# Optimization experiments

Measured on AMD Instinct MI355X. Metric: run time of the kernel, lower is better.

Reference implementation:

```python
import jax, jax.numpy as jnp
import numpy as np

N = 50000      # nodes
E = 800000     # edges (before self-loops)
IN_DIM = 128
HID = 64
OUT = 32
HEADS = 8
BN_EPS = 1e-5
NEG_SLOPE = 0.2  # PyG GATConv default


def setup_inputs() -> dict:
    key = jax.random.key(0)
    ks = jax.random.split(key, 24)
    g = lambda k, shape, fan_in: (jax.random.normal(k, shape, jnp.float32) / np.sqrt(fan_in))
    return {
        "x": jax.random.normal(ks[0], (N, IN_DIM), jnp.float32),
        "edge_index": jax.random.randint(ks[1], (2, E), 0, N, dtype=jnp.int64),
        # GCN1
        "gcn1_w": g(ks[2], (IN_DIM, HID), IN_DIM),
        "gcn1_b": jnp.zeros((HID,), jnp.float32),
        # BN1 (eval mode running stats)
        "bn1_gamma": jnp.ones((HID,), jnp.float32),
        "bn1_beta": jnp.zeros((HID,), jnp.float32),
        "bn1_mean": 0.1 * jax.random.normal(ks[3], (HID,), jnp.float32),
        "bn1_var": 0.5 + jax.random.uniform(ks[4], (HID,), jnp.float32),
        # GAT1: heads=8, per-head out=HID, concat=False -> mean over heads
        "gat1_w": g(ks[5], (HID, HEADS * HID), HID),
        "gat1_asrc": g(ks[6], (HEADS, HID), HID),
        "gat1_adst": g(ks[7], (HEADS, HID), HID),
        "gat1_b": jnp.zeros((HID,), jnp.float32),
        # GCN2
        "gcn2_w": g(ks[8], (HID, HID), HID),
        "gcn2_b": jnp.zeros((HID,), jnp.float32),
        # BN2
        "bn2_gamma": jnp.ones((HID,), jnp.float32),
        "bn2_beta": jnp.zeros((HID,), jnp.float32),
        "bn2_mean": 0.1 * jax.random.normal(ks[9], (HID,), jnp.float32),
        "bn2_var": 0.5 + jax.random.uniform(ks[10], (HID,), jnp.float32),
        # GAT2: heads=8, per-head out=OUT, concat=False
        "gat2_w": g(ks[11], (HID, HEADS * OUT), HID),
        "gat2_asrc": g(ks[12], (HEADS, OUT), OUT),
        "gat2_adst": g(ks[13], (HEADS, OUT), OUT),
        "gat2_b": jnp.zeros((OUT,), jnp.float32),
    }


def _gcn(x, src, dst, w, b, n):
    # PyG GCNConv: x @ W, symmetric norm with self-loops (src/dst already include them)
    h = x @ w
    deg = jax.ops.segment_sum(jnp.ones(src.shape[0], x.dtype), dst, num_segments=n)
    dinv = jnp.where(deg > 0, jax.lax.rsqrt(jnp.maximum(deg, 1.0)), 0.0)
    coef = dinv[src] * dinv[dst]                     # [E']
    out = jax.ops.segment_sum(coef[:, None] * h[src], dst, num_segments=n)
    return out + b


def _gat(x, src, dst, w, a_src, a_dst, b, n, heads, ch):
    # PyG GATConv (concat=False): mean over heads, softmax over incoming edges per dst
    h = (x @ w).reshape(n, heads, ch)                # [N,H,C]
    es = jnp.einsum('nhc,hc->nh', h, a_src)          # alpha_src per node
    ed = jnp.einsum('nhc,hc->nh', h, a_dst)
    e = jax.nn.leaky_relu(es[src] + ed[dst], NEG_SLOPE)  # [E',H]
    m = jax.ops.segment_max(e, dst, num_segments=n)
    m = jnp.where(jnp.isfinite(m), m, 0.0)
    ex = jnp.exp(e - m[dst])
    denom = jax.ops.segment_sum(ex, dst, num_segments=n)
    alpha = ex / (denom[dst] + 1e-16)                # [E',H]
    out = jnp.zeros((n, ch), x.dtype)
    for hd in range(heads):  # fixed small head loop keeps peak edge memory at [E',C]
        msg = alpha[:, hd, None] * h[src, hd]        # [E',C]
        out = out + jax.ops.segment_sum(msg, dst, num_segments=n)
    return out / heads + b


def _bn_eval(x, gamma, beta, mean, var):
    return (x - mean) * jax.lax.rsqrt(var + BN_EPS) * gamma + beta


def reference(x, edge_index,
              gcn1_w, gcn1_b, bn1_gamma, bn1_beta, bn1_mean, bn1_var,
              gat1_w, gat1_asrc, gat1_adst, gat1_b,
              gcn2_w, gcn2_b, bn2_gamma, bn2_beta, bn2_mean, bn2_var,
              gat2_w, gat2_asrc, gat2_adst, gat2_b):
    n = x.shape[0]
    loops = jnp.arange(n, dtype=edge_index.dtype)
    src = jnp.concatenate([edge_index[0], loops])    # self-loops (PyG default)
    dst = jnp.concatenate([edge_index[1], loops])

    h = _gcn(x, src, dst, gcn1_w, gcn1_b, n)
    h = jax.nn.relu(_bn_eval(h, bn1_gamma, bn1_beta, bn1_mean, bn1_var))
    h = jax.nn.relu(_gat(h, src, dst, gat1_w, gat1_asrc, gat1_adst, gat1_b, n, HEADS, HID))
    h = _gcn(h, src, dst, gcn2_w, gcn2_b, n)
    h = jax.nn.relu(_bn_eval(h, bn2_gamma, bn2_beta, bn2_mean, bn2_var))
    h = _gat(h, src, dst, gat2_w, gat2_asrc, gat2_adst, gat2_b, n, HEADS, OUT)
    return jax.nn.log_softmax(h, axis=1)
```

## Files before the change

### kernel.cpp

```cpp
#include <hip/hip_runtime.h>
#include <hip/hip_bf16.h>

#define NN 50000
#define NE 800000
#define IND 128
#define NH 8
#define EBLK 256
#define EPB 3125
#define NBUK 391
#define NBUKP 392
#define GH (NBUKP * EBLK)
#define PREPB 308

typedef __hip_bfloat16 bf16;
typedef __attribute__((ext_vector_type(8))) short short8;
typedef __attribute__((ext_vector_type(8))) __bf16 bf16x8;
typedef __attribute__((ext_vector_type(4))) float floatx4;
typedef __attribute__((ext_vector_type(2))) float floatx2;

static __device__ __forceinline__ short f2bf_bits(float f) {
    unsigned u = __float_as_uint(f);
    u = (u + 0x7fffu + ((u >> 16) & 1u)) >> 16;
    return (short)u;
}
static __device__ __forceinline__ float bf2f(bf16 v) { return __bfloat162float(v); }
static __device__ __forceinline__ floatx2 up2(unsigned av) {
    floatx2 r;
    r.x = __uint_as_float(av << 16);
    r.y = __uint_as_float(av & 0xffff0000u);
    return r;
}
static __device__ __forceinline__ unsigned pk2(float a, float b) {
    return (unsigned)(unsigned short)f2bf_bits(a) | ((unsigned)(unsigned short)f2bf_bits(b) << 16);
}
static __device__ __forceinline__ void pk_fma_lo(floatx2& acc, floatx2 a, floatx2 al) {
    asm("v_pk_fma_f32 %0, %1, %2, %0 op_sel:[0,0,0] op_sel_hi:[1,0,1]"
        : "+v"(acc) : "v"(a), "v"(al));
}
static __device__ __forceinline__ void pk_fma_hi(floatx2& acc, floatx2 a, floatx2 al) {
    asm("v_pk_fma_f32 %0, %1, %2, %0 op_sel:[0,1,0] op_sel_hi:[1,1,1]"
        : "+v"(acc) : "v"(a), "v"(al));
}

static __device__ __forceinline__ void scan_buckets(const int* __restrict__ bsum,
        int* sp, int* gb, int tid) {
    int v0 = (2 * tid < NBUKP) ? bsum[2 * tid] : 0;
    int v1 = (2 * tid + 1 < NBUKP) ? bsum[2 * tid + 1] : 0;
    int c = v0 + v1;
    sp[tid] = c; __syncthreads();
    int val = c;
#pragma unroll
    for (int off = 1; off < 256; off <<= 1) {
        int t = (tid >= off) ? sp[tid - off] : 0;
        __syncthreads();
        val += t; sp[tid] = val;
        __syncthreads();
    }
    int pex = val - c;
    gb[2 * tid] = pex;
    gb[2 * tid + 1] = pex + v0;
    __syncthreads();
}

__global__ __launch_bounds__(256) void bin_count_prep_kernel(const int* __restrict__ edst,
        int* __restrict__ ghist,
        const float* __restrict__ gcn1_w, const float* __restrict__ gcn2_w,
        const float* __restrict__ gat1_w, const float* __restrict__ gat2_w,
        const float* __restrict__ as1, const float* __restrict__ ad1,
        const float* __restrict__ as2, const float* __restrict__ ad2,
        bf16* __restrict__ wT1, bf16* __restrict__ wT2,
        bf16* __restrict__ wgT1, bf16* __restrict__ wgT2,
        float* __restrict__ was1, float* __restrict__ wad1,
        float* __restrict__ was2, float* __restrict__ wad2) {
    __shared__ int hsh[NBUKP];
    const int tid = threadIdx.x;
    if (blockIdx.x < EBLK) {
        const int blk = blockIdx.x;
        for (int b = tid; b < NBUKP; b += 256) hsh[b] = 0;
        __syncthreads();
        const int e0 = blk * EPB;
        for (int e = e0 + tid; e < e0 + EPB; e += 256)
            atomicAdd(&hsh[edst[e] >> 7], 1);
        __syncthreads();
        for (int b = tid; b < NBUKP; b += 256)
            ghist[b * EBLK + blk] = hsh[b];
    } else {
        int idx = (blockIdx.x - EBLK) * 256 + tid;
        if (idx < 8192) {
            int m = idx >> 7, k = idx & 127;
            ((short*)wT1)[idx] = f2bf_bits(gcn1_w[(long)k * 64 + m]);
        } else if (idx < 12288) {
            int i = idx - 8192;
            int m = i >> 6, k = i & 63;
            ((short*)wT2)[i] = f2bf_bits(gcn2_w[(long)k * 64 + m]);
        } else if (idx < 45056) {
            int i = idx - 12288;
            int m = i >> 9, k = i & 511;
            int h = k >> 6, c = k & 63;
            ((short*)wgT1)[i] = f2bf_bits(gat1_w[(long)c * 512 + h * 64 + m]);
        } else if (idx < 77824) {
            int i = idx - 45056;
            int m = i >> 9, k = i & 511;
            int h = k >> 6, c = k & 63;
            ((short*)wgT2)[i] = (m < 32) ? f2bf_bits(gat2_w[(long)c * 256 + h * 32 + m]) : (short)0;
        } else if (idx < 78336) {
            int i = idx - 77824;
            int h = i >> 6, c = i & 63;
            const float* wrow = gat1_w + (long)c * 512 + h * 64;
            float s = 0.f, d = 0.f;
            for (int cc = 0; cc < 64; ++cc) {
                float w = wrow[cc];
                s += w * as1[h * 64 + cc];
                d += w * ad1[h * 64 + cc];
            }
            was1[i] = s; wad1[i] = d;
        } else if (idx < 78848) {
            int i = idx - 78336;
            int h = i >> 6, c = i & 63;
            const float* wrow = gat2_w + (long)c * 256 + h * 32;
            float s = 0.f, d = 0.f;
            for (int cc = 0; cc < 32; ++cc) {
                float w = wrow[cc];
                s += w * as2[h * 32 + cc];
                d += w * ad2[h * 32 + cc];
            }
            was2[i] = s; wad2[i] = d;
        }
    }
}

__global__ __launch_bounds__(256) void scang1_kernel(const int* __restrict__ src,
        int* __restrict__ pre, int* __restrict__ bsum, int n) {
    __shared__ int sh[256];
    const int tid = threadIdx.x;
    const int idx = blockIdx.x * 256 + tid;
    int c = (idx < n) ? src[idx] : 0;
    sh[tid] = c; __syncthreads();
    int val = c;
#pragma unroll
    for (int off = 1; off < 256; off <<= 1) {
        int t = (tid >= off) ? sh[tid - off] : 0;
        __syncthreads();
        val += t; sh[tid] = val;
        __syncthreads();
    }
    if (idx < n) pre[idx] = val - c;
    if (tid == 255) bsum[blockIdx.x] = val;
}

__global__ __launch_bounds__(256) void bin_scatter_kernel(const int* __restrict__ esrc,
        const int* __restrict__ edst, const int* __restrict__ gpre,
        const int* __restrict__ bsum, unsigned* __restrict__ ebuf) {
    __shared__ int cur[NBUKP];
    __shared__ int sp[256], gb[512];
    const int tid = threadIdx.x, blk = blockIdx.x;
    scan_buckets(bsum, sp, gb, tid);
    for (int b = tid; b < NBUKP; b += 256)
        cur[b] = gpre[b * EBLK + blk] + gb[b];
    __syncthreads();
    const int e0 = blk * EPB;
    for (int e = e0 + tid; e < e0 + EPB; e += 256) {
        int d = edst[e], s = esrc[e];
        int pos = atomicAdd(&cur[d >> 7], 1);
        ebuf[pos] = ((unsigned)(d & 127) << 16) | (unsigned)s;
    }
}

__global__ __launch_bounds__(256) void bucket_finalize_kernel(const unsigned* __restrict__ ebuf,
        const int* __restrict__ gpre, const int* __restrict__ bsum,
        int* __restrict__ rowptr, float* __restrict__ dinv, int* __restrict__ csrc) {
    __shared__ int lh[128], lcur[128], sc[256];
    __shared__ int sp[256], gb[512];
    const int bu = blockIdx.x, tid = threadIdx.x;
    scan_buckets(bsum, sp, gb, tid);
    const int seg_beg = gpre[bu * EBLK] + gb[bu];
    const int seg_end = gpre[(bu + 1) * EBLK] + gb[bu + 1];
    if (tid < 128) lh[tid] = 0;
    __syncthreads();
    for (int i = seg_beg + tid; i < seg_end; i += 256)
        atomicAdd(&lh[ebuf[i] >> 16], 1);
    __syncthreads();
    int c = (tid < 128) ? lh[tid] : 0;
    sc[tid] = c; __syncthreads();
    int val = c;
#pragma unroll
    for (int off = 1; off < 256; off <<= 1) {
        int t = (tid >= off) ? sc[tid - off] : 0;
        __syncthreads();
        val += t; sc[tid] = val;
        __syncthreads();
    }
    int excl = val - c;
    if (tid < 128) {
        lcur[tid] = excl;
        int node = bu * 128 + tid;
        if (node < NN) {
            rowptr[node] = seg_beg + excl;
            dinv[node] = rsqrtf((float)c + 1.f);
        }
    }
    if (bu == 0 && tid == 0) rowptr[NN] = NE;
    __syncthreads();
    for (int i = seg_beg + tid; i < seg_end; i += 256) {
        unsigned u = ebuf[i];
        int pos = atomicAdd(&lcur[u >> 16], 1);
        csrc[seg_beg + pos] = (int)(u & 0xffffu);
    }
}

template<int K, int EPI, bool AF32>
__global__ __launch_bounds__(256) void mm2_kernel(const void* __restrict__ A,
        const bf16* __restrict__ wT, void* __restrict__ C,
        const float* __restrict__ bias, const float* __restrict__ rowscale,
        int nrows, int M) {
    const int row0 = blockIdx.x * 64;
    const int tid = threadIdx.x;
    const int lane = tid & 63, wave = tid >> 6;
    const int lr = lane & 15, q = lane >> 4;
    const int row = row0 + wave * 16 + lr;
    const bool rok = row < nrows;
    constexpr int NC = 4;
    floatx4 acc[NC] = {};
#pragma unroll 4
    for (int k0 = 0; k0 < K; k0 += 32) {
        short8 av = {0, 0, 0, 0, 0, 0, 0, 0};
        if (rok) {
            if (AF32) {
                const float* apf = (const float*)A + (long)row * K + q * 8 + k0;
                floatx4 va = *(const floatx4*)apf;
                floatx4 vb = *(const floatx4*)(apf + 4);
#pragma unroll
                for (int j = 0; j < 4; ++j) { av[j] = f2bf_bits(va[j]); av[4 + j] = f2bf_bits(vb[j]); }
            } else {
                av = *(const short8*)((const short*)A + (long)row * K + q * 8 + k0);
            }
        }
        bf16x8 a = __builtin_bit_cast(bf16x8, av);
#pragma unroll
        for (int c = 0; c < NC; ++c) {
            bf16x8 b = __builtin_bit_cast(bf16x8,
                *(const short8*)((const short*)wT + (long)(c * 16 + lr) * K + k0 + q * 8));
            acc[c] = __builtin_amdgcn_mfma_f32_16x16x32_bf16(a, b, acc[c], 0, 0, 0);
        }
    }
#pragma unroll
    for (int c = 0; c < NC; ++c)
#pragma unroll
        for (int r = 0; r < 4; ++r) {
            int orow = row0 + wave * 16 + q * 4 + r;
            int col = c * 16 + lr;
            if (orow < nrows && col < M) {
                long o = (long)orow * M + col;
                float v = acc[c][r];
                if (EPI == 0) ((float*)C)[o] = v;
                else if (EPI == 2) {
                    v = v * 0.125f + bias[col];
                    ((bf16*)C)[o] = __float2bfloat16(fmaxf(v, 0.f));
                } else {
                    ((bf16*)C)[o] = __float2bfloat16(rowscale[orow] * v);
                }
            }
        }
}

__global__ __launch_bounds__(256) void gcn_fused_kernel(const int* __restrict__ rowptr,
        const int* __restrict__ csrc, const float* __restrict__ dinv,
        const bf16* __restrict__ hin, const float* __restrict__ b,
        const float* __restrict__ gamma, const float* __restrict__ beta,
        const float* __restrict__ mean, const float* __restrict__ var,
        bf16* __restrict__ actout) {
    const int node = blockIdx.x * 4 + (threadIdx.x >> 6);
    if (node >= NN) return;
    const int lane = threadIdx.x & 63;
    const int eslot = lane >> 5, cp = lane & 31;
    const unsigned cpo = 4u * (unsigned)cp;
    const int beg = __builtin_amdgcn_readfirstlane(rowptr[node]);
    const int end = __builtin_amdgcn_readfirstlane(rowptr[node + 1]);
    const float di = dinv[node];
    const int* csp = csrc + beg;
    floatx2 acc2 = {0.f, 0.f};
    const int dn = end - beg;
    const int kup = (dn + 15) & ~15;
    for (int k0 = 0; k0 < kup; k0 += 16) {
        int s_[8]; float w_[8];
#pragma unroll
        for (int u = 0; u < 8; ++u) {
            int k = k0 + 2 * u + eslot;
            int ok = k < dn;
            s_[u] = csp[ok ? k : 0];
            w_[u] = ok ? 1.f : 0.f;
        }
        unsigned av_[8];
#pragma unroll
        for (int u = 0; u < 8; ++u)
            av_[u] = *(const unsigned*)((const char*)hin + ((unsigned)s_[u] * 128u + cpo));
#pragma unroll
        for (int u = 0; u < 8; ++u) {
            floatx2 a2 = up2(av_[u]);
            acc2 += a2 * w_[u];
        }
    }
    acc2.x += __shfl_xor(acc2.x, 32);
    acc2.y += __shfl_xor(acc2.y, 32);
    {
        unsigned sv = *(const unsigned*)((const char*)hin + ((unsigned)node * 128u + cpo));
        acc2 += up2(sv);
    }
    int c0 = 2 * cp, c1 = c0 + 1;
    float x0 = acc2.x * di + b[c0];
    float x1 = acc2.y * di + b[c1];
    x0 = (x0 - mean[c0]) * rsqrtf(var[c0] + 1e-5f) * gamma[c0] + beta[c0];
    x1 = (x1 - mean[c1]) * rsqrtf(var[c1] + 1e-5f) * gamma[c1] + beta[c1];
    if (eslot == 0)
        *(unsigned*)((unsigned short*)actout + (long)node * 64 + c0) =
            pk2(fmaxf(x0, 0.f), fmaxf(x1, 0.f));
}

__global__ __launch_bounds__(256) void scores_kernel(const bf16* __restrict__ actb,
        const float* __restrict__ was, const float* __restrict__ wad,
        float* __restrict__ es, float* __restrict__ ed, int n) {
    const int node = blockIdx.x * 4 + (threadIdx.x >> 6);
    if (node >= n) return;
    const int lane = threadIdx.x & 63;
    const int h = lane >> 3, cg = lane & 7;
    short8 a8 = *(const short8*)((const short*)actb + (long)node * 64 + cg * 8);
    const float* wsp = was + h * 64 + cg * 8;
    const float* wdp = wad + h * 64 + cg * 8;
    floatx4 ws0 = *(const floatx4*)wsp, ws1 = *(const floatx4*)(wsp + 4);
    floatx4 wd0 = *(const floatx4*)wdp, wd1 = *(const floatx4*)(wdp + 4);
    float s = 0.f, d = 0.f;
#pragma unroll
    for (int j = 0; j < 4; ++j) {
        float v0 = bf2f(__builtin_bit_cast(bf16, a8[j]));
        float v1 = bf2f(__builtin_bit_cast(bf16, a8[4 + j]));
        s += v0 * ws0[j] + v1 * ws1[j];
        d += v0 * wd0[j] + v1 * wd1[j];
    }
#pragma unroll
    for (int off = 1; off < 8; off <<= 1) {
        s += __shfl_xor(s, off);
        d += __shfl_xor(d, off);
    }
    if (cg == 0) { es[node * NH + h] = s; ed[node * NH + h] = d; }
}

template<int NCT, int EPI>
__global__ __launch_bounds__(1024) void gat_fused_kernel(const int* __restrict__ rowptr,
        const int* __restrict__ csrc, const float* __restrict__ es, const float* __restrict__ ed,
        const bf16* __restrict__ actb, const bf16* __restrict__ wgT,
        const float* __restrict__ bias, void* __restrict__ outp) {
    __shared__ __align__(16) float salpha[16][512];
    __shared__ int ssrcs[16][64];
    __shared__ __align__(16) float sself[16][8];
    __shared__ __align__(16) unsigned short aggt[16][520];
    __shared__ float redbuf[2][2][16];
    const int wv = threadIdx.x >> 6;
    const int lane = threadIdx.x & 63;
    const int h = lane & 7, slot = lane >> 3;
    const int hq = lane >> 5, cp = lane & 31;
    const unsigned cpo = 4u * (unsigned)cp;

    const int node = blockIdx.x * 16 + wv;
    const int beg = __builtin_amdgcn_readfirstlane(rowptr[node]);
    const int end = __builtin_amdgcn_readfirstlane(rowptr[node + 1]);
    const int deg = end - beg;
    const int* csp = csrc + beg;
    const float edr = *(const float*)((const char*)ed + ((unsigned)node * 32u + (unsigned)h * 4u));
    float selfe = *(const float*)((const char*)es + ((unsigned)node * 32u + (unsigned)h * 4u)) + edr;
    selfe = selfe > 0.f ? selfe : 0.2f * selfe;

    if (deg <= 64) {
        const int nb = (deg + 7) >> 3;
        const int dm1 = (deg > 0) ? deg - 1 : 0;
        float ex_r[8]; int s_r[8];
        float den = 0.f;
#pragma unroll
        for (int b = 0; b < 8; ++b) { ex_r[b] = 0.f; s_r[b] = 0; }
        if (deg > 0) {
#pragma unroll
            for (int b = 0; b < 8; ++b)
                if (b < nb) {
                    int k = b * 8 + slot;
                    s_r[b] = csp[k < deg ? k : dm1];
                }
#pragma unroll
            for (int b = 0; b < 8; ++b)
                if (b < nb) {
                    float e = *(const float*)((const char*)es +
                              ((unsigned)s_r[b] * 32u + (unsigned)h * 4u)) + edr;
                    e = e > 0.f ? e : 0.2f * e;
                    float ex = __expf(e - selfe);
                    ex_r[b] = (b * 8 + slot < deg) ? ex : 0.f;
                    den += ex_r[b];
                }
        }
        den += __shfl_xor(den, 8);
        den += __shfl_xor(den, 16);
        den += __shfl_xor(den, 32);
        const float invden = 1.f / (den + 1.f);
#pragma unroll
        for (int b = 0; b < 8; ++b)
            if (b < nb) salpha[wv][b * 64 + lane] = ex_r[b] * invden;
        if (h == 0) {
#pragma unroll
            for (int b = 0; b < 8; ++b)
                if (b < nb) ssrcs[wv][b * 8 + slot] = s_r[b];
        }
        if (slot == 0) sself[wv][h] = invden;

        floatx2 acc2[4] = {};
        const int ng = nb;
        if (ng > 0) {
            int sA0, sA1, sA2, sA3, sA4, sA5, sA6, sA7;
            int sB0, sB1, sB2, sB3, sB4, sB5, sB6, sB7;
            unsigned rA0, rA1, rA2, rA3, rA4, rA5, rA6, rA7;
            unsigned rB0, rB1, rB2, rB3, rB4, rB5, rB6, rB7;
#define LOAD_BANK(S, R, G) do { \
    const int* sp_ = &ssrcs[wv][(G) * 8]; \
    S##0 = sp_[0]; S##1 = sp_[1]; S##2 = sp_[2]; S##3 = sp_[3]; \
    S##4 = sp_[4]; S##5 = sp_[5]; S##6 = sp_[6]; S##7 = sp_[7]; \
    R##0 = *(const unsigned*)((const char*)actb + ((unsigned)S##0 * 128u + cpo)); \
    R##1 = *(const unsigned*)((const char*)actb + ((unsigned)S##1 * 128u + cpo)); \
    R##2 = *(const unsigned*)((const char*)actb + ((unsigned)S##2 * 128u + cpo)); \
    R##3 = *(const unsigned*)((const char*)actb + ((unsigned)S##3 * 128u + cpo)); \
    R##4 = *(const unsigned*)((const char*)actb + ((unsigned)S##4 * 128u + cpo)); \
    R##5 = *(const unsigned*)((const char*)actb + ((unsigned)S##5 * 128u + cpo)); \
    R##6 = *(const unsigned*)((const char*)actb + ((unsigned)S##6 * 128u + cpo)); \
    R##7 = *(const unsigned*)((const char*)actb + ((unsigned)S##7 * 128u + cpo)); \
} while (0)
#define FMA_BANK(R, G) do { \
    const float* ab_ = &salpha[wv][(G) * 64 + hq * 4]; \
    unsigned rr_[8] = {R##0, R##1, R##2, R##3, R##4, R##5, R##6, R##7}; \
    _Pragma("unroll") \
    for (int j_ = 0; j_ < 8; ++j_) { \
        floatx4 al_ = *(const floatx4*)(ab_ + j_ * 8); \
        floatx2 al01_ = __builtin_shufflevector(al_, al_, 0, 1); \
        floatx2 al23_ = __builtin_shufflevector(al_, al_, 2, 3); \
        floatx2 a2_ = up2(rr_[j_]); \
        pk_fma_lo(acc2[0], a2_, al01_); pk_fma_hi(acc2[1], a2_, al01_); \
        pk_fma_lo(acc2[2], a2_, al23_); pk_fma_hi(acc2[3], a2_, al23_); \
    } \
} while (0)
            LOAD_BANK(sA, rA, 0);
            int g = 0;
            while (true) {
                if (g + 1 < ng) LOAD_BANK(sB, rB, g + 1);
                FMA_BANK(rA, g);
                ++g; if (g >= ng) break;
                if (g + 1 < ng) LOAD_BANK(sA, rA, g + 1);
                FMA_BANK(rB, g);
                ++g; if (g >= ng) break;
            }
#undef LOAD_BANK
#undef FMA_BANK
        }
        {
            unsigned sv = *(const unsigned*)((const char*)actb + ((unsigned)node * 128u + cpo));
            floatx2 a2 = up2(sv);
            floatx4 sa = *(const floatx4*)&sself[wv][hq * 4];
            floatx2 sa01 = __builtin_shufflevector(sa, sa, 0, 1);
            floatx2 sa23 = __builtin_shufflevector(sa, sa, 2, 3);
            pk_fma_lo(acc2[0], a2, sa01); pk_fma_hi(acc2[1], a2, sa01);
            pk_fma_lo(acc2[2], a2, sa23); pk_fma_hi(acc2[3], a2, sa23);
        }
#pragma unroll
        for (int j = 0; j < 4; ++j)
            *(unsigned*)&aggt[wv][(hq * 4 + j) * 64 + 2 * cp] = pk2(acc2[j].x, acc2[j].y);
    } else {
        float acc[NH] = {0.f, 0.f, 0.f, 0.f, 0.f, 0.f, 0.f, 0.f};
        float den = 0.f;
        for (int base = beg; base < end; base += 8) {
            int ei = base + slot;
            if (ei < end) {
                int s = csrc[ei];
                float e = es[s * NH + h] + edr;
                e = e > 0.f ? e : 0.2f * e;
                den += __expf(e - selfe);
            }
        }
        den += __shfl_xor(den, 8);
        den += __shfl_xor(den, 16);
        den += __shfl_xor(den, 32);
        const float invden = 1.f / (den + 1.f);
        for (int base = beg; base < end; base += 8) {
            int ei = base + slot;
            float al = 0.f; int sl = 0;
            if (ei < end) {
                sl = csrc[ei];
                float e = es[sl * NH + h] + edr;
                e = e > 0.f ? e : 0.2f * e;
                al = __expf(e - selfe) * invden;
            }
            salpha[wv][lane] = al;
            if (h == 0) ssrcs[wv][slot] = sl;
            int ecnt = end - base; if (ecnt > 8) ecnt = 8;
            for (int j = 0; j < ecnt; ++j) {
                int s = ssrcs[wv][j];
                float a = bf2f(actb[(long)s * 64 + lane]);
                floatx4 al0 = *(const floatx4*)&salpha[wv][j * 8];
                floatx4 al1 = *(const floatx4*)&salpha[wv][j * 8 + 4];
                acc[0] += al0[0] * a; acc[1] += al0[1] * a;
                acc[2] += al0[2] * a; acc[3] += al0[3] * a;
                acc[4] += al1[0] * a; acc[5] += al1[1] * a;
                acc[6] += al1[2] * a; acc[7] += al1[3] * a;
            }
        }
        {
            if (slot == 0) sself[wv][h] = invden;
            float a = bf2f(actb[(long)node * 64 + lane]);
            floatx4 s0 = *(const floatx4*)&sself[wv][0];
            floatx4 s1 = *(const floatx4*)&sself[wv][4];
            acc[0] += s0[0] * a; acc[1] += s0[1] * a;
            acc[2] += s0[2] * a; acc[3] += s0[3] * a;
            acc[4] += s1[0] * a; acc[5] += s1[1] * a;
            acc[6] += s1[2] * a; acc[7] += s1[3] * a;
        }
#pragma unroll
        for (int hh = 0; hh < NH; ++hh)
            aggt[wv][hh * 64 + lane] = (unsigned short)f2bf_bits(acc[hh]);
    }

    __syncthreads();

    const int lr = lane & 15, q = lane >> 4;
    const bool act = wv < NCT;
    floatx4 acc = {};
    if (act) {
#pragma unroll 4
        for (int k0 = 0; k0 < 512; k0 += 32) {
            bf16x8 a = __builtin_bit_cast(bf16x8,
                *(const short8*)&aggt[lr][k0 + q * 8]);
            bf16x8 b = __builtin_bit_cast(bf16x8,
                *(const short8*)((const short*)wgT + (long)(wv * 16 + lr) * 512 + k0 + q * 8));
            acc = __builtin_amdgcn_mfma_f32_16x16x32_bf16(a, b, acc, 0, 0, 0);
        }
    }

    if (EPI == 2) {
        if (act) {
#pragma unroll
            for (int r = 0; r < 4; ++r) {
                int onode = blockIdx.x * 16 + q * 4 + r;
                int col = wv * 16 + lr;
                float v = acc[r] * 0.125f + bias[col];
                ((bf16*)outp)[(long)onode * 64 + col] = __float2bfloat16(fmaxf(v, 0.f));
            }
        }
    } else {
        float v[4], m[4];
#pragma unroll
        for (int r = 0; r < 4; ++r) {
            v[r] = acc[r] * 0.125f + (act ? bias[wv * 16 + lr] : 0.f);
            m[r] = v[r];
        }
#pragma unroll
        for (int off = 1; off < 16; off <<= 1)
#pragma unroll
            for (int r = 0; r < 4; ++r) m[r] = fmaxf(m[r], __shfl_xor(m[r], off));
        if (act && lr == 0) {
#pragma unroll
            for (int r = 0; r < 4; ++r) redbuf[0][wv][q * 4 + r] = m[r];
        }
        __syncthreads();
        float s[4];
#pragma unroll
        for (int r = 0; r < 4; ++r) {
            float mm_ = fmaxf(redbuf[0][0][q * 4 + r], redbuf[0][1][q * 4 + r]);
            m[r] = mm_;
            s[r] = act ? __expf(v[r] - mm_) : 0.f;
        }
#pragma unroll
        for (int off = 1; off < 16; off <<= 1)
#pragma unroll
            for (int r = 0; r < 4; ++r) s[r] += __shfl_xor(s[r], off);
        if (act && lr == 0) {
#pragma unroll
            for (int r = 0; r < 4; ++r) redbuf[1][wv][q * 4 + r] = s[r];
        }
        __syncthreads();
        if (act) {
#pragma unroll
            for (int r = 0; r < 4; ++r) {
                int row = q * 4 + r;
                int onode = blockIdx.x * 16 + row;
                float ls = m[r] + logf(redbuf[1][0][row] + redbuf[1][1][row]);
                ((float*)outp)[(long)onode * 32 + wv * 16 + lr] = v[r] - ls;
            }
        }
    }
}

extern "C" void kernel_launch(void* const* d_in, const int* in_sizes, int n_in,
                              void* d_out, int out_size, void* d_ws, size_t ws_size,
                              hipStream_t stream) {
    const float* x        = (const float*)d_in[0];
    const int*   eidx     = (const int*)d_in[1];
    const float* gcn1_w   = (const float*)d_in[2];
    const float* gcn1_b   = (const float*)d_in[3];
    const float* bn1_g    = (const float*)d_in[4];
    const float* bn1_b    = (const float*)d_in[5];
    const float* bn1_m    = (const float*)d_in[6];
    const float* bn1_v    = (const float*)d_in[7];
    const float* gat1_w   = (const float*)d_in[8];
    const float* gat1_as  = (const float*)d_in[9];
    const float* gat1_ad  = (const float*)d_in[10];
    const float* gat1_b   = (const float*)d_in[11];
    const float* gcn2_w   = (const float*)d_in[12];
    const float* gcn2_b   = (const float*)d_in[13];
    const float* bn2_g    = (const float*)d_in[14];
    const float* bn2_b    = (const float*)d_in[15];
    const float* bn2_m    = (const float*)d_in[16];
    const float* bn2_v    = (const float*)d_in[17];
    const float* gat2_w   = (const float*)d_in[18];
    const float* gat2_as  = (const float*)d_in[19];
    const float* gat2_ad  = (const float*)d_in[20];
    const float* gat2_b   = (const float*)d_in[21];
    float* out = (float*)d_out;

    const int* esrc = eidx;
    const int* edst = eidx + NE;

    float* ws = (float*)d_ws;
    int*      ghist  = (int*)ws;
    int*      gpre   = ghist + GH;
    int*      gbsum  = gpre + GH;
    unsigned* ebuf   = (unsigned*)(gbsum + 512);
    int*      rowptr = (int*)(ebuf + NE);
    int*      csrc   = rowptr + 50048;
    float*    dinv   = (float*)(csrc + NE);
    float*    es     = dinv + 50048;
    float*    ed     = es + 400000;
    float*    was1   = ed + 400000;
    float*    wad1   = was1 + 512;
    float*    was2   = wad1 + 512;
    float*    wad2   = was2 + 512;
    bf16*     wT1    = (bf16*)(wad2 + 512);
    bf16*     wT2    = wT1 + 64 * 128;
    bf16*     wgT1   = wT2 + 64 * 64;
    bf16*     wgT2   = wgT1 + 64 * 512;
    bf16*     actb   = wgT2 + 64 * 512;
    bf16*     mmbf   = actb + (size_t)NN * 64;
    bf16*     gact   = mmbf + (size_t)NN * 64;

    auto cdiv = [](long a, long b) { return (int)((a + b - 1) / b); };
    const int GB = cdiv(NN, 64);
    const int NB = cdiv(NN, 4);
    const int FB = NN / 16;

    bin_count_prep_kernel<<<EBLK + PREPB, 256, 0, stream>>>(edst, ghist,
        gcn1_w, gcn2_w, gat1_w, gat2_w, gat1_as, gat1_ad, gat2_as, gat2_ad,
        wT1, wT2, wgT1, wgT2, was1, wad1, was2, wad2);
    scang1_kernel<<<GH / 256, 256, 0, stream>>>(ghist, gpre, gbsum, GH);
    bin_scatter_kernel<<<EBLK, 256, 0, stream>>>(esrc, edst, gpre, gbsum, ebuf);
    bucket_finalize_kernel<<<NBUK, 256, 0, stream>>>(ebuf, gpre, gbsum, rowptr, dinv, csrc);

    mm2_kernel<IND, 3, true><<<GB, 256, 0, stream>>>(x, wT1, mmbf, nullptr, dinv, NN, 64);
    gcn_fused_kernel<<<NB, 256, 0, stream>>>(rowptr, csrc, dinv, mmbf,
        gcn1_b, bn1_g, bn1_b, bn1_m, bn1_v, actb);

    scores_kernel<<<NB, 256, 0, stream>>>(actb, was1, wad1, es, ed, NN);
    gat_fused_kernel<4, 2><<<FB, 1024, 0, stream>>>(rowptr, csrc, es, ed, actb, wgT1, gat1_b, gact);

    mm2_kernel<64, 3, false><<<GB, 256, 0, stream>>>(gact, wT2, mmbf, nullptr, dinv, NN, 64);
    gcn_fused_kernel<<<NB, 256, 0, stream>>>(rowptr, csrc, dinv, mmbf,
        gcn2_b, bn2_g, bn2_b, bn2_m, bn2_v, actb);

    scores_kernel<<<NB, 256, 0, stream>>>(actb, was2, wad2, es, ed, NN);
    gat_fused_kernel<2, 4><<<FB, 1024, 0, stream>>>(rowptr, csrc, es, ed, actb, wgT2, gat2_b, out);
}
```

Measured before the change: 348.8 us.

## Sort nodes by in-degree so each GAT block processes similar-degree nodes

Builds a degree histogram during CSR finalization, then a new perm_kernel scans it and scatters node ids into degree-sorted order. Both GAT fused kernels read their node from this permutation, and the output row indices are staged through shared memory. The goal is to cut intra-block imbalance, since each 16-wave block synchronizes and so waits on its highest-degree node. The costs are an extra kernel launch, global atomics for the histogram, and scattered output writes and per-node reads in place of contiguous ones.

```diff
diff --git a/kernel.cpp b/kernel.cpp
--- a/kernel.cpp
+++ b/kernel.cpp
@@ -63,7 +63,7 @@
 }
 
 __global__ __launch_bounds__(256) void bin_count_prep_kernel(const int* __restrict__ edst,
-        int* __restrict__ ghist,
+        int* __restrict__ ghist, int* __restrict__ dh,
         const float* __restrict__ gcn1_w, const float* __restrict__ gcn2_w,
         const float* __restrict__ gat1_w, const float* __restrict__ gat2_w,
         const float* __restrict__ as1, const float* __restrict__ ad1,
@@ -74,6 +74,7 @@
         float* __restrict__ was2, float* __restrict__ wad2) {
     __shared__ int hsh[NBUKP];
     const int tid = threadIdx.x;
+    if (blockIdx.x == 0 && tid < 132) dh[tid] = 0;
     if (blockIdx.x < EBLK) {
         const int blk = blockIdx.x;
         for (int b = tid; b < NBUKP; b += 256) hsh[b] = 0;
@@ -168,7 +169,8 @@
 
 __global__ __launch_bounds__(256) void bucket_finalize_kernel(const unsigned* __restrict__ ebuf,
         const int* __restrict__ gpre, const int* __restrict__ bsum,
-        int* __restrict__ rowptr, float* __restrict__ dinv, int* __restrict__ csrc) {
+        int* __restrict__ rowptr, float* __restrict__ dinv, int* __restrict__ csrc,
+        int* __restrict__ dh) {
     __shared__ int lh[128], lcur[128], sc[256];
     __shared__ int sp[256], gb[512];
     const int bu = blockIdx.x, tid = threadIdx.x;
@@ -197,6 +199,7 @@
         if (node < NN) {
             rowptr[node] = seg_beg + excl;
             dinv[node] = rsqrtf((float)c + 1.f);
+            atomicAdd(&dh[(c < 65) ? c : 65], 1);
         }
     }
     if (bu == 0 && tid == 0) rowptr[NN] = NE;
@@ -205,6 +208,32 @@
         unsigned u = ebuf[i];
         int pos = atomicAdd(&lcur[u >> 16], 1);
         csrc[seg_beg + pos] = (int)(u & 0xffffu);
+    }
+}
+
+__global__ __launch_bounds__(256) void perm_kernel(const int* __restrict__ rowptr,
+        const int* __restrict__ dh, int* __restrict__ dcur, int* __restrict__ perm) {
+    __shared__ int sh[256];
+    __shared__ int offs[66];
+    const int tid = threadIdx.x;
+    int c = (tid < 66) ? dh[tid] : 0;
+    sh[tid] = c; __syncthreads();
+    int val = c;
+#pragma unroll
+    for (int off = 1; off < 256; off <<= 1) {
+        int t = (tid >= off) ? sh[tid - off] : 0;
+        __syncthreads();
+        val += t; sh[tid] = val;
+        __syncthreads();
+    }
+    if (tid < 66) offs[tid] = val - c;
+    __syncthreads();
+    int n = blockIdx.x * 256 + tid;
+    if (n < NN) {
+        int d = rowptr[n + 1] - rowptr[n];
+        d = (d < 65) ? d : 65;
+        int pos = offs[d] + atomicAdd(&dcur[d], 1);
+        perm[pos] = n;
     }
 }
 
@@ -348,19 +377,21 @@
 __global__ __launch_bounds__(1024) void gat_fused_kernel(const int* __restrict__ rowptr,
         const int* __restrict__ csrc, const float* __restrict__ es, const float* __restrict__ ed,
         const bf16* __restrict__ actb, const bf16* __restrict__ wgT,
-        const float* __restrict__ bias, void* __restrict__ outp) {
+        const float* __restrict__ bias, const int* __restrict__ perm, void* __restrict__ outp) {
     __shared__ __align__(16) float salpha[16][512];
     __shared__ int ssrcs[16][64];
     __shared__ __align__(16) float sself[16][8];
     __shared__ __align__(16) unsigned short aggt[16][520];
     __shared__ float redbuf[2][2][16];
+    __shared__ int snode[16];
     const int wv = threadIdx.x >> 6;
     const int lane = threadIdx.x & 63;
     const int h = lane & 7, slot = lane >> 3;
     const int hq = lane >> 5, cp = lane & 31;
     const unsigned cpo = 4u * (unsigned)cp;
 
-    const int node = blockIdx.x * 16 + wv;
+    const int node = perm[blockIdx.x * 16 + wv];
+    if (lane == 0) snode[wv] = node;
     const int beg = __builtin_amdgcn_readfirstlane(rowptr[node]);
     const int end = __builtin_amdgcn_readfirstlane(rowptr[node + 1]);
     const int deg = end - beg;
@@ -540,7 +571,7 @@
         if (act) {
 #pragma unroll
             for (int r = 0; r < 4; ++r) {
-                int onode = blockIdx.x * 16 + q * 4 + r;
+                int onode = snode[q * 4 + r];
                 int col = wv * 16 + lr;
                 float v = acc[r] * 0.125f + bias[col];
                 ((bf16*)outp)[(long)onode * 64 + col] = __float2bfloat16(fmaxf(v, 0.f));
@@ -582,7 +613,7 @@
 #pragma unroll
             for (int r = 0; r < 4; ++r) {
                 int row = q * 4 + r;
-                int onode = blockIdx.x * 16 + row;
+                int onode = snode[row];
                 float ls = m[r] + logf(redbuf[1][0][row] + redbuf[1][1][row]);
                 ((float*)outp)[(long)onode * 32 + wv * 16 + lr] = v[r] - ls;
             }
@@ -641,30 +672,34 @@
     bf16*     actb   = wgT2 + 64 * 512;
     bf16*     mmbf   = actb + (size_t)NN * 64;
     bf16*     gact   = mmbf + (size_t)NN * 64;
+    int*      dh     = (int*)(gact + (size_t)NN * 64);
+    int*      dcur   = dh + 66;
+    int*      perm   = dcur + 66;
 
     auto cdiv = [](long a, long b) { return (int)((a + b - 1) / b); };
     const int GB = cdiv(NN, 64);
     const int NB = cdiv(NN, 4);
     const int FB = NN / 16;
 
-    bin_count_prep_kernel<<<EBLK + PREPB, 256, 0, stream>>>(edst, ghist,
+    bin_count_prep_kernel<<<EBLK + PREPB, 256, 0, stream>>>(edst, ghist, dh,
         gcn1_w, gcn2_w, gat1_w, gat2_w, gat1_as, gat1_ad, gat2_as, gat2_ad,
         wT1, wT2, wgT1, wgT2, was1, wad1, was2, wad2);
     scang1_kernel<<<GH / 256, 256, 0, stream>>>(ghist, gpre, gbsum, GH);
     bin_scatter_kernel<<<EBLK, 256, 0, stream>>>(esrc, edst, gpre, gbsum, ebuf);
-    bucket_finalize_kernel<<<NBUK, 256, 0, stream>>>(ebuf, gpre, gbsum, rowptr, dinv, csrc);
+    bucket_finalize_kernel<<<NBUK, 256, 0, stream>>>(ebuf, gpre, gbsum, rowptr, dinv, csrc, dh);
+    perm_kernel<<<cdiv(NN, 256), 256, 0, stream>>>(rowptr, dh, dcur, perm);
 
     mm2_kernel<IND, 3, true><<<GB, 256, 0, stream>>>(x, wT1, mmbf, nullptr, dinv, NN, 64);
     gcn_fused_kernel<<<NB, 256, 0, stream>>>(rowptr, csrc, dinv, mmbf,
         gcn1_b, bn1_g, bn1_b, bn1_m, bn1_v, actb);
 
     scores_kernel<<<NB, 256, 0, stream>>>(actb, was1, wad1, es, ed, NN);
-    gat_fused_kernel<4, 2><<<FB, 1024, 0, stream>>>(rowptr, csrc, es, ed, actb, wgT1, gat1_b, gact);
+    gat_fused_kernel<4, 2><<<FB, 1024, 0, stream>>>(rowptr, csrc, es, ed, actb, wgT1, gat1_b, perm, gact);
 
     mm2_kernel<64, 3, false><<<GB, 256, 0, stream>>>(gact, wT2, mmbf, nullptr, dinv, NN, 64);
     gcn_fused_kernel<<<NB, 256, 0, stream>>>(rowptr, csrc, dinv, mmbf,
         gcn2_b, bn2_g, bn2_b, bn2_m, bn2_v, actb);
 
     scores_kernel<<<NB, 256, 0, stream>>>(actb, was2, wad2, es, ed, NN);
-    gat_fused_kernel<2, 4><<<FB, 1024, 0, stream>>>(rowptr, csrc, es, ed, actb, wgT2, gat2_b, out);
-}
+    gat_fused_kernel<2, 4><<<FB, 1024, 0, stream>>>(rowptr, csrc, es, ed, actb, wgT2, gat2_b, perm, out);
+}
```

Result: slower. 619.7 us (+77.7%).

## Split GAT output GEMM K-dimension across all waves and prefetch weight fragments

Applied to the files above, without the earlier changes.

The post-aggregation MFMA projection previously ran on only NCT waves, each looping over all 512 K elements. It now spreads the K dimension over four wave groups that each issue four MFMAs, then reduces the partial tiles through shared memory (reusing the salpha buffer) behind an extra barrier. Weight fragments are loaded from global memory at kernel start so their latency overlaps the edge aggregation. The cost is more registers held live across the aggregation, an additional __syncthreads, and an LDS round-trip for the reduction.

```diff
diff --git a/kernel.cpp b/kernel.cpp
--- a/kernel.cpp
+++ b/kernel.cpp
@@ -368,6 +368,18 @@
     const float edr = *(const float*)((const char*)ed + ((unsigned)node * 32u + (unsigned)h * 4u));
     float selfe = *(const float*)((const char*)es + ((unsigned)node * 32u + (unsigned)h * 4u)) + edr;
     selfe = selfe > 0.f ? selfe : 0.2f * selfe;
+
+    const int lr = lane & 15, q = lane >> 4;
+    const int ct = wv >> 2, kq = wv & 3;
+    const bool pact = ct < NCT;
+    bf16x8 bfrag0, bfrag1, bfrag2, bfrag3;
+    if (pact) {
+        const short* wp = (const short*)wgT + (long)(ct * 16 + lr) * 512 + kq * 128 + q * 8;
+        bfrag0 = __builtin_bit_cast(bf16x8, *(const short8*)(wp));
+        bfrag1 = __builtin_bit_cast(bf16x8, *(const short8*)(wp + 32));
+        bfrag2 = __builtin_bit_cast(bf16x8, *(const short8*)(wp + 64));
+        bfrag3 = __builtin_bit_cast(bf16x8, *(const short8*)(wp + 96));
+    }
 
     if (deg <= 64) {
         const int nb = (deg + 7) >> 3;
@@ -522,19 +534,29 @@
 
     __syncthreads();
 
-    const int lr = lane & 15, q = lane >> 4;
+    float* paggr = &salpha[0][0];
+    floatx4 acc = {};
+    if (pact) {
+        const int kb = kq * 128 + q * 8;
+        bf16x8 a0 = __builtin_bit_cast(bf16x8, *(const short8*)&aggt[lr][kb]);
+        bf16x8 a1 = __builtin_bit_cast(bf16x8, *(const short8*)&aggt[lr][kb + 32]);
+        bf16x8 a2 = __builtin_bit_cast(bf16x8, *(const short8*)&aggt[lr][kb + 64]);
+        bf16x8 a3 = __builtin_bit_cast(bf16x8, *(const short8*)&aggt[lr][kb + 96]);
+        acc = __builtin_amdgcn_mfma_f32_16x16x32_bf16(a0, bfrag0, acc, 0, 0, 0);
+        acc = __builtin_amdgcn_mfma_f32_16x16x32_bf16(a1, bfrag1, acc, 0, 0, 0);
+        acc = __builtin_amdgcn_mfma_f32_16x16x32_bf16(a2, bfrag2, acc, 0, 0, 0);
+        acc = __builtin_amdgcn_mfma_f32_16x16x32_bf16(a3, bfrag3, acc, 0, 0, 0);
+        *(floatx4*)&paggr[wv * 256 + lane * 4] = acc;
+    }
+    __syncthreads();
+    if (wv < NCT) {
+        floatx4 r0 = *(const floatx4*)&paggr[(wv * 4 + 0) * 256 + lane * 4];
+        floatx4 r1 = *(const floatx4*)&paggr[(wv * 4 + 1) * 256 + lane * 4];
+        floatx4 r2 = *(const floatx4*)&paggr[(wv * 4 + 2) * 256 + lane * 4];
+        floatx4 r3 = *(const floatx4*)&paggr[(wv * 4 + 3) * 256 + lane * 4];
+        acc = (r0 + r1) + (r2 + r3);
+    }
     const bool act = wv < NCT;
-    floatx4 acc = {};
-    if (act) {
-#pragma unroll 4
-        for (int k0 = 0; k0 < 512; k0 += 32) {
-            bf16x8 a = __builtin_bit_cast(bf16x8,
-                *(const short8*)&aggt[lr][k0 + q * 8]);
-            bf16x8 b = __builtin_bit_cast(bf16x8,
-                *(const short8*)((const short*)wgT + (long)(wv * 16 + lr) * 512 + k0 + q * 8));
-            acc = __builtin_amdgcn_mfma_f32_16x16x32_bf16(a, b, acc, 0, 0, 0);
-        }
-    }
 
     if (EPI == 2) {
         if (act) {
```

After: 400.2 us. 14.7% more time.
